# Optimization experiments

Measured on AMD Instinct MI355X. Metric: run time of the kernel, lower is better.

The kernel has to match this reference:

```python
import math
import jax, jax.numpy as jnp
import numpy as np

V_NODES = 100000
N_EDGES = 1600000
EMBED = 768
HID = 256
H = 4
FH = HID // H
L = 2
PE_D = EMBED // 4  # 192
SLOPE = 0.2


def make_pe(max_len, d):
    pos = np.arange(max_len, dtype=np.float32)[:, None]
    div = np.exp(np.arange(0, d, 2, dtype=np.float32) * (-math.log(10000.0) / d))
    pe = np.zeros((max_len, d), dtype=np.float32)
    pe[:, 0::2] = np.sin(pos * div)
    pe[:, 1::2] = np.cos(pos * div)
    return jnp.asarray(pe)


def setup_inputs() -> dict:
    key = jax.random.key(0)
    ks = jax.random.split(key, 24)

    def xavier(k, shape):
        fan_in, fan_out = shape[0], shape[1]
        lim = math.sqrt(6.0 / (fan_in + fan_out))
        return jax.random.uniform(k, shape, jnp.float32, -lim, lim)

    in_proj_dim = EMBED + 2 * PE_D  # 1152
    inp = {
        'row_idx': jax.random.randint(ks[0], (V_NODES,), 0, 256),
        'col_idx': jax.random.randint(ks[1], (V_NODES,), 0, 64),
        'edge_index': jax.random.randint(ks[2], (2, N_EDGES), 0, V_NODES),
        'edge_weight': jax.random.uniform(ks[3], (N_EDGES,), jnp.float32),
        'W_in': xavier(ks[4], (in_proj_dim, HID)),
        'b_in': jnp.zeros((HID,), jnp.float32),
        'ln_g': jnp.ones((HID,), jnp.float32),
        'ln_b': jnp.zeros((HID,), jnp.float32),
        'Wq': jnp.stack([xavier(ks[5 + i], (HID, HID)) for i in range(L)]),
        'bq': jnp.zeros((L, HID), jnp.float32),
        'Wk': jnp.stack([xavier(ks[7 + i], (HID, HID)) for i in range(L)]),
        'bk': jnp.zeros((L, HID), jnp.float32),
        'Wv': jnp.stack([xavier(ks[9 + i], (HID, HID)) for i in range(L)]),
        'bv': jnp.zeros((L, HID), jnp.float32),
        'Wo': jnp.stack([xavier(ks[11 + i], (HID, HID)) for i in range(L)]),
        'bo': jnp.zeros((L, HID), jnp.float32),
        'We': jnp.stack([xavier(ks[13 + i], (1, H)) for i in range(L)]),  # edge_proj weight [1,H]
        'be': jnp.zeros((L, H), jnp.float32),
    }
    return inp


def gat_layer(h, src, tgt, ew, Wq, bq, Wk, bk, Wv, bv, Wo, bo, We, be):
    V = h.shape[0]
    Q = (h @ Wq + bq).reshape(V, H, FH)
    K = (h @ Wk + bk).reshape(V, H, FH)
    Vo = (h @ Wv + bv).reshape(V, H, FH)
    # edge bias: Linear(1,H) on edge_weight, then leaky relu -> [E,H]
    edge_bias = jax.nn.leaky_relu(ew[:, None] * We.reshape(1, H) + be, SLOPE)
    attn_raw = jnp.sum(Q[src] * K[tgt], axis=-1) / math.sqrt(FH) + edge_bias  # [E,H]
    attn_exp = jnp.exp(attn_raw)
    deg = jax.ops.segment_sum(attn_exp, tgt, num_segments=V) + 1e-16  # [V,H]
    attn_norm = attn_exp / deg[tgt]  # [E,H] (dropout is identity at eval)
    msg = Vo[src] * attn_norm[:, :, None] * ew[:, None, None]  # [E,H,FH]
    out = jax.ops.segment_sum(msg, tgt, num_segments=V).reshape(V, H * FH)
    return jax.nn.leaky_relu(out @ Wo + bo, SLOPE)


def reference(row_idx, col_idx, edge_index, edge_weight,
              W_in, b_in, ln_g, ln_b,
              Wq, bq, Wk, bk, Wv, bv, Wo, bo, We, be):
    V = row_idx.shape[0]
    row_pe = make_pe(256, PE_D)
    col_pe = make_pe(64, PE_D)
    cell = jnp.zeros((V, EMBED), jnp.float32)  # cell_embeds are zeros in source
    h = jnp.concatenate([cell, row_pe[row_idx], col_pe[col_idx]], axis=-1)
    # input_proj: Linear -> LayerNorm -> ReLU (dropout identity)
    h = h @ W_in + b_in
    mu = jnp.mean(h, axis=-1, keepdims=True)
    var = jnp.var(h, axis=-1, keepdims=True)
    h = (h - mu) / jnp.sqrt(var + 1e-5) * ln_g + ln_b
    h = jax.nn.relu(h)
    src, tgt = edge_index[0], edge_index[1]
    for i in range(L):
        h = gat_layer(h, src, tgt, edge_weight,
                      Wq[i], bq[i], Wk[i], bk[i], Wv[i], bv[i],
                      Wo[i], bo[i], We[i], be[i])
    return h
```

## Files before the change

kernel.cpp:

```cpp
#include <hip/hip_runtime.h>
#include <hip/hip_bf16.h>
#include <type_traits>
#include <math.h>

typedef __attribute__((ext_vector_type(8))) short bf16x8;
typedef __attribute__((ext_vector_type(4))) float f32x4;

typedef __attribute__((address_space(3))) char       lds_char;
typedef const __attribute__((address_space(1))) char g_char;

__device__ __forceinline__ float bf2f(unsigned int u16) {
    union { unsigned int i; float f; } x; x.i = (u16 & 0xffffu) << 16; return x.f;
}
__device__ __forceinline__ unsigned int f2bf(float f) {
    union { float f; unsigned int i; } x; x.f = f;
    unsigned int i = x.i;
    unsigned int r = i + 0x7fffu + ((i >> 16) & 1u);
    return r >> 16;
}

#define SLOPE 0.2f

__global__ void k_hist(const int* __restrict__ tgt, int* __restrict__ cnt, int E) {
    int i = blockIdx.x * blockDim.x + threadIdx.x;
    if (i < E) atomicAdd(&cnt[tgt[i]], 1);
}

__global__ void __launch_bounds__(1024) k_scan1(const int* __restrict__ in, int* __restrict__ out,
                                                int* __restrict__ bsums, int n) {
    __shared__ int sm[1024];
    int i = blockIdx.x * 1024 + threadIdx.x;
    int v = (i < n) ? in[i] : 0;
    sm[threadIdx.x] = v; __syncthreads();
    for (int ofs = 1; ofs < 1024; ofs <<= 1) {
        int t = (threadIdx.x >= ofs) ? sm[threadIdx.x - ofs] : 0;
        __syncthreads();
        sm[threadIdx.x] += t;
        __syncthreads();
    }
    if (i < n) out[i] = sm[threadIdx.x];
    if (threadIdx.x == 1023) bsums[blockIdx.x] = sm[1023];
}

__global__ void __launch_bounds__(1024) k_scan2(int* bsums, int nb) {
    __shared__ int sm[1024];
    int v = (threadIdx.x < nb) ? bsums[threadIdx.x] : 0;
    sm[threadIdx.x] = v; __syncthreads();
    for (int ofs = 1; ofs < 1024; ofs <<= 1) {
        int t = (threadIdx.x >= ofs) ? sm[threadIdx.x - ofs] : 0;
        __syncthreads();
        sm[threadIdx.x] += t;
        __syncthreads();
    }
    if (threadIdx.x < nb) bsums[threadIdx.x] = sm[threadIdx.x] - v;
}

__global__ void __launch_bounds__(1024) k_scan3(int* __restrict__ out1, const int* __restrict__ bsums,
                                                int* __restrict__ off0, int n) {
    int i = blockIdx.x * 1024 + threadIdx.x;
    if (i < n) out1[i] += bsums[blockIdx.x];
    if (i == 0) off0[0] = 0;
}

__global__ void k_combo(const int* __restrict__ ri, const int* __restrict__ ci,
                        int* __restrict__ combo, int V) {
    int v = blockIdx.x * blockDim.x + threadIdx.x;
    if (v < V) combo[v] = ri[v] * 64 + ci[v];
}

__global__ void k_scatter(const int* __restrict__ ei, const float* __restrict__ ew,
                          const int* __restrict__ off, int* __restrict__ fill,
                          int2* __restrict__ p, int E) {
    int e = blockIdx.x * blockDim.x + threadIdx.x;
    if (e < E) {
        int s = ei[e], t = ei[E + e];
        int pos = off[t] + atomicAdd(&fill[t], 1);
        p[pos] = make_int2(s, __float_as_int(ew[e]));
    }
}

__global__ void __launch_bounds__(256) k_wt(const float* __restrict__ Wq, const float* __restrict__ Wk,
                                            const float* __restrict__ Wv, const float* __restrict__ Wo,
                                            unsigned short* __restrict__ WT) {
    __shared__ float sm[64][65];
    int blk = blockIdx.x;
    int m = blk >> 4, t = blk & 15;
    int tr = t >> 2, tc = t & 3;
    const float* srcs[4] = {Wq, Wk, Wv, Wo};
    const float* W = srcs[m & 3] + (size_t)(m >> 2) * 65536;
    int tid = threadIdx.x;
    for (int i = tid; i < 4096; i += 256) {
        int r = i >> 6, c = i & 63;
        sm[r][c] = W[(size_t)(tr * 64 + r) * 256 + tc * 64 + c];
    }
    __syncthreads();
    for (int i = tid; i < 4096; i += 256) {
        int n = i >> 6, k = i & 63;
        WT[(size_t)(m * 256 + tc * 64 + n) * 256 + tr * 64 + k] = (unsigned short)f2bf(sm[k][n]);
    }
}

__global__ void __launch_bounds__(256) k_bias(const float* __restrict__ bq, const float* __restrict__ bk,
                                              const float* __restrict__ bv, const float* __restrict__ bo,
                                              float* __restrict__ biasF) {
    int m = blockIdx.x, n = threadIdx.x;
    const float* srcs[4] = {bq, bk, bv, bo};
    biasF[m * 256 + n] = srcs[m & 3][(m >> 2) * 256 + n];
}

__global__ void __launch_bounds__(256) k_peproj(const float* __restrict__ W_in, float* __restrict__ AB) {
    __shared__ float pe[192];
    int blk = blockIdx.x;
    bool isA = blk < 256;
    int pos = isA ? blk : blk - 256;
    const float* Wb = W_in + (size_t)(isA ? 768 : 960) * 256;
    int tid = threadIdx.x;
    if (tid < 192) {
        float div = expf(-(float)(tid & ~1) * (logf(10000.0f) / 192.0f));
        float ang = (float)pos * div;
        pe[tid] = (tid & 1) ? cosf(ang) : sinf(ang);
    }
    __syncthreads();
    float acc = 0.f;
    #pragma unroll 8
    for (int d = 0; d < 192; ++d) acc = fmaf(pe[d], Wb[d * 256 + tid], acc);
    AB[blk * 256 + tid] = acc;
}

__global__ void __launch_bounds__(256) k_h0(const float* __restrict__ AB, const float* __restrict__ b_in,
                                            const float* __restrict__ g, const float* __restrict__ b,
                                            unsigned short* __restrict__ h0t) {
    int wid = threadIdx.x >> 6, lane = threadIdx.x & 63;
    int m = blockIdx.x * 4 + wid;
    int r = m >> 6, c = m & 63;
    float4 a  = ((const float4*)(AB + (size_t)r * 256))[lane];
    float4 bb = ((const float4*)(AB + (size_t)(256 + c) * 256))[lane];
    float4 bi = ((const float4*)b_in)[lane];
    float x0 = a.x + bb.x + bi.x, x1 = a.y + bb.y + bi.y;
    float x2 = a.z + bb.z + bi.z, x3 = a.w + bb.w + bi.w;
    float s = x0 + x1 + x2 + x3;
    #pragma unroll
    for (int msk = 1; msk < 64; msk <<= 1) s += __shfl_xor(s, msk);
    float mu = s * (1.f / 256.f);
    float d0 = x0 - mu, d1 = x1 - mu, d2 = x2 - mu, d3 = x3 - mu;
    float sq = d0 * d0 + d1 * d1 + d2 * d2 + d3 * d3;
    #pragma unroll
    for (int msk = 1; msk < 64; msk <<= 1) sq += __shfl_xor(sq, msk);
    float rstd = rsqrtf(sq * (1.f / 256.f) + 1e-5f);
    float4 gv = ((const float4*)g)[lane], bv = ((const float4*)b)[lane];
    float y0 = fmaxf(fmaf(d0 * rstd, gv.x, bv.x), 0.f);
    float y1 = fmaxf(fmaf(d1 * rstd, gv.y, bv.y), 0.f);
    float y2 = fmaxf(fmaf(d2 * rstd, gv.z, bv.z), 0.f);
    float y3 = fmaxf(fmaf(d3 * rstd, gv.w, bv.w), 0.f);
    uint2 o;
    o.x = f2bf(y0) | (f2bf(y1) << 16);
    o.y = f2bf(y2) | (f2bf(y3) << 16);
    *(uint2*)(h0t + (size_t)m * 256 + lane * 4) = o;
}

template <typename TC, bool LEAKY>
__global__ void __launch_bounds__(256) k_mm(const unsigned short* __restrict__ A,
                                            const unsigned short* __restrict__ WT,
                                            const float* __restrict__ bias,
                                            TC* __restrict__ C, int M, int ldc) {
    __shared__ __align__(16) char AsB[16384];
    __shared__ __align__(16) char BsB[16384];
    int tid = threadIdx.x;
    int R0 = blockIdx.x * 128, C0 = blockIdx.y * 128;
    int lane = tid & 63, wave = tid >> 6;
    int wr = (wave >> 1) * 64, wc = (wave & 1) * 64;
    int fr = lane & 15, fq = lane >> 4;
    f32x4 acc[4][4] = {};
    for (int k0 = 0; k0 < 256; k0 += 64) {
        #pragma unroll
        for (int it = 0; it < 4; ++it) {
            int chunk = it * 256 + tid;
            int r = chunk >> 3, cb = (chunk & 7) * 16;
            int sc = cb ^ ((r & 7) << 4);
            int gr = R0 + r;
            if (gr < M)
                __builtin_amdgcn_global_load_lds(
                    (g_char*)((const char*)(A + (size_t)gr * 256 + k0) + sc),
                    (lds_char*)(AsB + (size_t)(it * 256 + wave * 64) * 16), 16, 0, 0);
            __builtin_amdgcn_global_load_lds(
                (g_char*)((const char*)(WT + (size_t)(C0 + r) * 256 + k0) + sc),
                (lds_char*)(BsB + (size_t)(it * 256 + wave * 64) * 16), 16, 0, 0);
        }
        __syncthreads();
        #pragma unroll
        for (int ks = 0; ks < 2; ++ks) {
            bf16x8 af[4], bfv[4];
            #pragma unroll
            for (int mi = 0; mi < 4; ++mi) {
                int r = wr + mi * 16 + fr;
                int kb = ks * 64 + fq * 16;
                af[mi] = *(const bf16x8*)(AsB + r * 128 + (kb ^ ((r & 7) << 4)));
            }
            #pragma unroll
            for (int ni = 0; ni < 4; ++ni) {
                int r = wc + ni * 16 + fr;
                int kb = ks * 64 + fq * 16;
                bfv[ni] = *(const bf16x8*)(BsB + r * 128 + (kb ^ ((r & 7) << 4)));
            }
            #pragma unroll
            for (int mi = 0; mi < 4; ++mi)
                #pragma unroll
                for (int ni = 0; ni < 4; ++ni)
                    acc[mi][ni] = __builtin_amdgcn_mfma_f32_16x16x32_bf16(af[mi], bfv[ni], acc[mi][ni], 0, 0, 0);
        }
        __syncthreads();
    }
    #pragma unroll
    for (int mi = 0; mi < 4; ++mi) {
        #pragma unroll
        for (int r = 0; r < 4; ++r) {
            int row = R0 + wr + mi * 16 + fq * 4 + r;
            if (row >= M) continue;
            #pragma unroll
            for (int ni = 0; ni < 4; ++ni) {
                int col = C0 + wc + ni * 16 + fr;
                float v = acc[mi][ni][r] + bias[col];
                if (LEAKY) v = fmaxf(v, SLOPE * v);
                if constexpr (std::is_same<TC, float>::value) {
                    C[(size_t)row * ldc + col] = v;
                } else {
                    C[(size_t)row * ldc + col] = (unsigned short)f2bf(v);
                }
            }
        }
    }
}

template <bool USE_COMBO>
__global__ void __launch_bounds__(256) k_edge(const int* __restrict__ off, const int2* __restrict__ pedge,
                                              const int* __restrict__ combo,
                                              const unsigned short* __restrict__ QKV,
                                              const float* __restrict__ We_l, const float* __restrict__ be_l,
                                              unsigned short* __restrict__ out, int V) {
    int wid = threadIdx.x >> 6, lane = threadIdx.x & 63;
    int t = blockIdx.x * 4 + wid;
    if (t >= V) return;
    int q = lane & 15, quarter = lane >> 4;
    int h = q >> 2;
    int krow = USE_COMBO ? combo[t] : t;
    uint4 ka = *(const uint4*)(QKV + (size_t)krow * 768 + 256 + q * 16);
    uint4 kb = *(const uint4*)(QKV + (size_t)krow * 768 + 256 + q * 16 + 8);
    float kf[16];
    kf[0] = bf2f(ka.x); kf[1] = bf2f(ka.x >> 16); kf[2] = bf2f(ka.y); kf[3] = bf2f(ka.y >> 16);
    kf[4] = bf2f(ka.z); kf[5] = bf2f(ka.z >> 16); kf[6] = bf2f(ka.w); kf[7] = bf2f(ka.w >> 16);
    kf[8] = bf2f(kb.x); kf[9] = bf2f(kb.x >> 16); kf[10] = bf2f(kb.y); kf[11] = bf2f(kb.y >> 16);
    kf[12] = bf2f(kb.z); kf[13] = bf2f(kb.z >> 16); kf[14] = bf2f(kb.w); kf[15] = bf2f(kb.w >> 16);
    float Weh = We_l[h], beh = be_l[h];
    float n[16];
    #pragma unroll
    for (int j = 0; j < 16; ++j) n[j] = 0.f;
    float den = 0.f;
    int beg = off[t], end = off[t + 1];
    for (int e0 = beg; e0 < end; e0 += 64) {
        int nrem = end - e0; if (nrem > 64) nrem = 64;
        int sv = 0; float wv = 0.f;
        if (lane < nrem) {
            int2 pr = pedge[e0 + lane];
            sv = pr.x;
            wv = __int_as_float(pr.y);
            if (USE_COMBO) sv = combo[sv];
        }
        for (int i = 0; i < nrem; i += 4) {
            int ei = i + quarter;
            bool act = ei < nrem;
            int eidx = act ? ei : (nrem - 1);
            int srow = __shfl(sv, eidx);
            float w  = __shfl(wv, eidx);
            const unsigned short* base = QKV + (size_t)srow * 768 + q * 16;
            uint4 qa = *(const uint4*)base;
            uint4 qb = *(const uint4*)(base + 8);
            uint4 va = *(const uint4*)(base + 512);
            uint4 vb = *(const uint4*)(base + 520);
            float p;
            p = bf2f(qa.x) * kf[0];
            p = fmaf(bf2f(qa.x >> 16), kf[1], p);
            p = fmaf(bf2f(qa.y),       kf[2], p);
            p = fmaf(bf2f(qa.y >> 16), kf[3], p);
            p = fmaf(bf2f(qa.z),       kf[4], p);
            p = fmaf(bf2f(qa.z >> 16), kf[5], p);
            p = fmaf(bf2f(qa.w),       kf[6], p);
            p = fmaf(bf2f(qa.w >> 16), kf[7], p);
            p = fmaf(bf2f(qb.x),       kf[8], p);
            p = fmaf(bf2f(qb.x >> 16), kf[9], p);
            p = fmaf(bf2f(qb.y),       kf[10], p);
            p = fmaf(bf2f(qb.y >> 16), kf[11], p);
            p = fmaf(bf2f(qb.z),       kf[12], p);
            p = fmaf(bf2f(qb.z >> 16), kf[13], p);
            p = fmaf(bf2f(qb.w),       kf[14], p);
            p = fmaf(bf2f(qb.w >> 16), kf[15], p);
            p += __shfl_xor(p, 1);
            p += __shfl_xor(p, 2);
            float bias = fmaf(w, Weh, beh);
            bias = fmaxf(bias, SLOPE * bias);
            float ex = act ? __expf(fmaf(p, 0.125f, bias)) : 0.f;
            den += ex;
            float cc = ex * w;
            n[0]  = fmaf(cc, bf2f(va.x),       n[0]);
            n[1]  = fmaf(cc, bf2f(va.x >> 16), n[1]);
            n[2]  = fmaf(cc, bf2f(va.y),       n[2]);
            n[3]  = fmaf(cc, bf2f(va.y >> 16), n[3]);
            n[4]  = fmaf(cc, bf2f(va.z),       n[4]);
            n[5]  = fmaf(cc, bf2f(va.z >> 16), n[5]);
            n[6]  = fmaf(cc, bf2f(va.w),       n[6]);
            n[7]  = fmaf(cc, bf2f(va.w >> 16), n[7]);
            n[8]  = fmaf(cc, bf2f(vb.x),       n[8]);
            n[9]  = fmaf(cc, bf2f(vb.x >> 16), n[9]);
            n[10] = fmaf(cc, bf2f(vb.y),       n[10]);
            n[11] = fmaf(cc, bf2f(vb.y >> 16), n[11]);
            n[12] = fmaf(cc, bf2f(vb.z),       n[12]);
            n[13] = fmaf(cc, bf2f(vb.z >> 16), n[13]);
            n[14] = fmaf(cc, bf2f(vb.w),       n[14]);
            n[15] = fmaf(cc, bf2f(vb.w >> 16), n[15]);
        }
    }
    den += __shfl_xor(den, 16);
    den += __shfl_xor(den, 32);
    #pragma unroll
    for (int j = 0; j < 16; ++j) {
        n[j] += __shfl_xor(n[j], 16);
        n[j] += __shfl_xor(n[j], 32);
    }
    float inv = 1.f / (den + 1e-16f);
    if (quarter == 0) {
        uint4 o0, o1;
        o0.x = f2bf(n[0] * inv)  | (f2bf(n[1] * inv) << 16);
        o0.y = f2bf(n[2] * inv)  | (f2bf(n[3] * inv) << 16);
        o0.z = f2bf(n[4] * inv)  | (f2bf(n[5] * inv) << 16);
        o0.w = f2bf(n[6] * inv)  | (f2bf(n[7] * inv) << 16);
        o1.x = f2bf(n[8] * inv)  | (f2bf(n[9] * inv) << 16);
        o1.y = f2bf(n[10] * inv) | (f2bf(n[11] * inv) << 16);
        o1.z = f2bf(n[12] * inv) | (f2bf(n[13] * inv) << 16);
        o1.w = f2bf(n[14] * inv) | (f2bf(n[15] * inv) << 16);
        *(uint4*)(out + (size_t)t * 256 + q * 16) = o0;
        *(uint4*)(out + (size_t)t * 256 + q * 16 + 8) = o1;
    }
}

extern "C" void kernel_launch(void* const* d_in, const int* in_sizes, int n_in,
                              void* d_out, int out_size, void* d_ws, size_t ws_size,
                              hipStream_t stream) {
    const int*   row_idx = (const int*)d_in[0];
    const int*   col_idx = (const int*)d_in[1];
    const int*   ei      = (const int*)d_in[2];
    const float* ew      = (const float*)d_in[3];
    const float* W_in    = (const float*)d_in[4];
    const float* b_in    = (const float*)d_in[5];
    const float* ln_g    = (const float*)d_in[6];
    const float* ln_b    = (const float*)d_in[7];
    const float* Wq      = (const float*)d_in[8];
    const float* bq      = (const float*)d_in[9];
    const float* Wk      = (const float*)d_in[10];
    const float* bk      = (const float*)d_in[11];
    const float* Wv      = (const float*)d_in[12];
    const float* bv      = (const float*)d_in[13];
    const float* Wo      = (const float*)d_in[14];
    const float* bo      = (const float*)d_in[15];
    const float* We      = (const float*)d_in[16];
    const float* be      = (const float*)d_in[17];

    const int V = in_sizes[0];
    const int E = in_sizes[3];
    const int NC = 16384;

    char* w = (char*)d_ws;
    size_t o = 0;
    auto alloc = [&](size_t bytes) -> char* {
        char* p = w + o;
        o = (o + bytes + 255) & ~(size_t)255;
        return p;
    };
    int*   cnt     = (int*)alloc((size_t)V * 4);
    int*   fill    = (int*)alloc((size_t)V * 4);
    int*   csr_off = (int*)alloc((size_t)(V + 1) * 4);
    int*   bsums   = (int*)alloc(1024 * 4);
    int2*  csrP    = (int2*)alloc((size_t)E * 8);
    int*   combo   = (int*)alloc((size_t)V * 4);
    float* AB      = (float*)alloc((size_t)320 * 256 * 4);
    unsigned short* WT    = (unsigned short*)alloc((size_t)2048 * 256 * 2);
    float*          biasF = (float*)alloc((size_t)2048 * 4);
    unsigned short* h0t   = (unsigned short*)alloc((size_t)NC * 256 * 2);
    unsigned short* QKV1  = (unsigned short*)alloc((size_t)NC * 768 * 2);
    unsigned short* out_e = (unsigned short*)alloc((size_t)V * 256 * 2);
    unsigned short* h1    = (unsigned short*)alloc((size_t)V * 256 * 2);
    unsigned short* QKV2  = (unsigned short*)alloc((size_t)V * 768 * 2);

    hipMemsetAsync(cnt, 0, (size_t)V * 4, stream);
    hipMemsetAsync(fill, 0, (size_t)V * 4, stream);

    int eb = (E + 255) / 256;
    int nscan = (V + 1023) / 1024;
    k_hist<<<eb, 256, 0, stream>>>(ei + E, cnt, E);
    k_scan1<<<nscan, 1024, 0, stream>>>(cnt, csr_off + 1, bsums, V);
    k_scan2<<<1, 1024, 0, stream>>>(bsums, nscan);
    k_scan3<<<nscan, 1024, 0, stream>>>(csr_off + 1, bsums, csr_off, V);
    k_combo<<<(V + 255) / 256, 256, 0, stream>>>(row_idx, col_idx, combo, V);
    k_scatter<<<eb, 256, 0, stream>>>(ei, ew, csr_off, fill, csrP, E);

    k_wt<<<128, 256, 0, stream>>>(Wq, Wk, Wv, Wo, WT);
    k_bias<<<8, 256, 0, stream>>>(bq, bk, bv, bo, biasF);
    k_peproj<<<320, 256, 0, stream>>>(W_in, AB);
    k_h0<<<NC / 4, 256, 0, stream>>>(AB, b_in, ln_g, ln_b, h0t);

    dim3 g1(NC / 128, 6);
    k_mm<unsigned short, false><<<g1, 256, 0, stream>>>(h0t, WT, biasF, QKV1, NC, 768);

    int tb = (V + 3) / 4;
    k_edge<true><<<tb, 256, 0, stream>>>(csr_off, csrP, combo, QKV1, We, be, out_e, V);

    int mb = (V + 127) / 128;
    dim3 go(mb, 2);
    dim3 gqkv(mb, 6);
    k_mm<unsigned short, true><<<go, 256, 0, stream>>>(out_e, WT + (size_t)768 * 256, biasF + 768, h1, V, 256);
    k_mm<unsigned short, false><<<gqkv, 256, 0, stream>>>(h1, WT + (size_t)1024 * 256, biasF + 1024, QKV2, V, 768);

    k_edge<false><<<tb, 256, 0, stream>>>(csr_off, csrP, combo, QKV2, We + 4, be + 4, out_e, V);

    k_mm<float, true><<<go, 256, 0, stream>>>(out_e, WT + (size_t)1792 * 256, biasF + 1792, (float*)d_out, V, 256);
}
```

Measured before the change: 788.6 us.

## Merge setup kernels into one prep launch and use 256-row GEMM tiles

Folds the weight transpose, bias copy, positional-encoding projection and combo-index kernels into a single multi-role prep kernel, and merges the two memsets into one. It also adds a 512-thread GEMM variant that covers 256 rows per block so each B tile loaded into LDS serves twice as many rows, and uses it for the three full-V matmuls. The single memset relies on cnt and fill sitting next to each other in the allocator, and the larger tile uses more LDS per block, which can lower occupancy.

```diff
diff --git a/kernel.cpp b/kernel.cpp
--- a/kernel.cpp
+++ b/kernel.cpp
@@ -62,12 +62,6 @@
     if (i == 0) off0[0] = 0;
 }
 
-__global__ void k_combo(const int* __restrict__ ri, const int* __restrict__ ci,
-                        int* __restrict__ combo, int V) {
-    int v = blockIdx.x * blockDim.x + threadIdx.x;
-    if (v < V) combo[v] = ri[v] * 64 + ci[v];
-}
-
 __global__ void k_scatter(const int* __restrict__ ei, const float* __restrict__ ew,
                           const int* __restrict__ off, int* __restrict__ fill,
                           int2* __restrict__ p, int E) {
@@ -79,52 +73,56 @@
     }
 }
 
-__global__ void __launch_bounds__(256) k_wt(const float* __restrict__ Wq, const float* __restrict__ Wk,
-                                            const float* __restrict__ Wv, const float* __restrict__ Wo,
-                                            unsigned short* __restrict__ WT) {
+__global__ void __launch_bounds__(256) k_prep(const float* __restrict__ Wq, const float* __restrict__ Wk,
+                                              const float* __restrict__ Wv, const float* __restrict__ Wo,
+                                              unsigned short* __restrict__ WT,
+                                              const float* __restrict__ bq, const float* __restrict__ bk,
+                                              const float* __restrict__ bv, const float* __restrict__ bo,
+                                              float* __restrict__ biasF,
+                                              const float* __restrict__ W_in, float* __restrict__ AB,
+                                              const int* __restrict__ ri, const int* __restrict__ ci,
+                                              int* __restrict__ combo, int V) {
     __shared__ float sm[64][65];
     int blk = blockIdx.x;
-    int m = blk >> 4, t = blk & 15;
-    int tr = t >> 2, tc = t & 3;
-    const float* srcs[4] = {Wq, Wk, Wv, Wo};
-    const float* W = srcs[m & 3] + (size_t)(m >> 2) * 65536;
     int tid = threadIdx.x;
-    for (int i = tid; i < 4096; i += 256) {
-        int r = i >> 6, c = i & 63;
-        sm[r][c] = W[(size_t)(tr * 64 + r) * 256 + tc * 64 + c];
-    }
-    __syncthreads();
-    for (int i = tid; i < 4096; i += 256) {
-        int n = i >> 6, k = i & 63;
-        WT[(size_t)(m * 256 + tc * 64 + n) * 256 + tr * 64 + k] = (unsigned short)f2bf(sm[k][n]);
-    }
-}
-
-__global__ void __launch_bounds__(256) k_bias(const float* __restrict__ bq, const float* __restrict__ bk,
-                                              const float* __restrict__ bv, const float* __restrict__ bo,
-                                              float* __restrict__ biasF) {
-    int m = blockIdx.x, n = threadIdx.x;
-    const float* srcs[4] = {bq, bk, bv, bo};
-    biasF[m * 256 + n] = srcs[m & 3][(m >> 2) * 256 + n];
-}
-
-__global__ void __launch_bounds__(256) k_peproj(const float* __restrict__ W_in, float* __restrict__ AB) {
-    __shared__ float pe[192];
-    int blk = blockIdx.x;
-    bool isA = blk < 256;
-    int pos = isA ? blk : blk - 256;
-    const float* Wb = W_in + (size_t)(isA ? 768 : 960) * 256;
-    int tid = threadIdx.x;
-    if (tid < 192) {
-        float div = expf(-(float)(tid & ~1) * (logf(10000.0f) / 192.0f));
-        float ang = (float)pos * div;
-        pe[tid] = (tid & 1) ? cosf(ang) : sinf(ang);
-    }
-    __syncthreads();
-    float acc = 0.f;
-    #pragma unroll 8
-    for (int d = 0; d < 192; ++d) acc = fmaf(pe[d], Wb[d * 256 + tid], acc);
-    AB[blk * 256 + tid] = acc;
+    if (blk < 128) {
+        int m = blk >> 4, t = blk & 15;
+        int tr = t >> 2, tc = t & 3;
+        const float* srcs[4] = {Wq, Wk, Wv, Wo};
+        const float* W = srcs[m & 3] + (size_t)(m >> 2) * 65536;
+        for (int i = tid; i < 4096; i += 256) {
+            int r = i >> 6, c = i & 63;
+            sm[r][c] = W[(size_t)(tr * 64 + r) * 256 + tc * 64 + c];
+        }
+        __syncthreads();
+        for (int i = tid; i < 4096; i += 256) {
+            int n = i >> 6, k = i & 63;
+            WT[(size_t)(m * 256 + tc * 64 + n) * 256 + tr * 64 + k] = (unsigned short)f2bf(sm[k][n]);
+        }
+    } else if (blk < 136) {
+        int m = blk - 128;
+        const float* srcs[4] = {bq, bk, bv, bo};
+        biasF[m * 256 + tid] = srcs[m & 3][(m >> 2) * 256 + tid];
+    } else if (blk < 456) {
+        int b2 = blk - 136;
+        bool isA = b2 < 256;
+        int pos = isA ? b2 : b2 - 256;
+        const float* Wb = W_in + (size_t)(isA ? 768 : 960) * 256;
+        float* pe = &sm[0][0];
+        if (tid < 192) {
+            float div = expf(-(float)(tid & ~1) * (logf(10000.0f) / 192.0f));
+            float ang = (float)pos * div;
+            pe[tid] = (tid & 1) ? cosf(ang) : sinf(ang);
+        }
+        __syncthreads();
+        float acc = 0.f;
+        #pragma unroll 8
+        for (int d = 0; d < 192; ++d) acc = fmaf(pe[d], Wb[d * 256 + tid], acc);
+        AB[b2 * 256 + tid] = acc;
+    } else {
+        int v = (blk - 456) * 256 + tid;
+        if (v < V) combo[v] = ri[v] * 64 + ci[v];
+    }
 }
 
 __global__ void __launch_bounds__(256) k_h0(const float* __restrict__ AB, const float* __restrict__ b_in,
@@ -185,6 +183,85 @@
             __builtin_amdgcn_global_load_lds(
                 (g_char*)((const char*)(WT + (size_t)(C0 + r) * 256 + k0) + sc),
                 (lds_char*)(BsB + (size_t)(it * 256 + wave * 64) * 16), 16, 0, 0);
+        }
+        __syncthreads();
+        #pragma unroll
+        for (int ks = 0; ks < 2; ++ks) {
+            bf16x8 af[4], bfv[4];
+            #pragma unroll
+            for (int mi = 0; mi < 4; ++mi) {
+                int r = wr + mi * 16 + fr;
+                int kb = ks * 64 + fq * 16;
+                af[mi] = *(const bf16x8*)(AsB + r * 128 + (kb ^ ((r & 7) << 4)));
+            }
+            #pragma unroll
+            for (int ni = 0; ni < 4; ++ni) {
+                int r = wc + ni * 16 + fr;
+                int kb = ks * 64 + fq * 16;
+                bfv[ni] = *(const bf16x8*)(BsB + r * 128 + (kb ^ ((r & 7) << 4)));
+            }
+            #pragma unroll
+            for (int mi = 0; mi < 4; ++mi)
+                #pragma unroll
+                for (int ni = 0; ni < 4; ++ni)
+                    acc[mi][ni] = __builtin_amdgcn_mfma_f32_16x16x32_bf16(af[mi], bfv[ni], acc[mi][ni], 0, 0, 0);
+        }
+        __syncthreads();
+    }
+    #pragma unroll
+    for (int mi = 0; mi < 4; ++mi) {
+        #pragma unroll
+        for (int r = 0; r < 4; ++r) {
+            int row = R0 + wr + mi * 16 + fq * 4 + r;
+            if (row >= M) continue;
+            #pragma unroll
+            for (int ni = 0; ni < 4; ++ni) {
+                int col = C0 + wc + ni * 16 + fr;
+                float v = acc[mi][ni][r] + bias[col];
+                if (LEAKY) v = fmaxf(v, SLOPE * v);
+                if constexpr (std::is_same<TC, float>::value) {
+                    C[(size_t)row * ldc + col] = v;
+                } else {
+                    C[(size_t)row * ldc + col] = (unsigned short)f2bf(v);
+                }
+            }
+        }
+    }
+}
+
+template <typename TC, bool LEAKY>
+__global__ void __launch_bounds__(512) k_mm256(const unsigned short* __restrict__ A,
+                                               const unsigned short* __restrict__ WT,
+                                               const float* __restrict__ bias,
+                                               TC* __restrict__ C, int M, int ldc) {
+    __shared__ __align__(16) char AsB[32768];
+    __shared__ __align__(16) char BsB[16384];
+    int tid = threadIdx.x;
+    int lane = tid & 63, wave = tid >> 6;
+    int R0 = blockIdx.x * 256, C0 = blockIdx.y * 128;
+    int wr = (wave >> 1) * 64, wc = (wave & 1) * 64;
+    int fr = lane & 15, fq = lane >> 4;
+    f32x4 acc[4][4] = {};
+    for (int k0 = 0; k0 < 256; k0 += 64) {
+        #pragma unroll
+        for (int it = 0; it < 4; ++it) {
+            int chunk = it * 512 + tid;
+            int r = chunk >> 3, cb = (chunk & 7) * 16;
+            int sc = cb ^ ((r & 7) << 4);
+            int gr = R0 + r;
+            if (gr < M)
+                __builtin_amdgcn_global_load_lds(
+                    (g_char*)((const char*)(A + (size_t)gr * 256 + k0) + sc),
+                    (lds_char*)(AsB + (size_t)(it * 512 + wave * 64) * 16), 16, 0, 0);
+        }
+        #pragma unroll
+        for (int it = 0; it < 2; ++it) {
+            int chunk = it * 512 + tid;
+            int r = chunk >> 3, cb = (chunk & 7) * 16;
+            int sc = cb ^ ((r & 7) << 4);
+            __builtin_amdgcn_global_load_lds(
+                (g_char*)((const char*)(WT + (size_t)(C0 + r) * 256 + k0) + sc),
+                (lds_char*)(BsB + (size_t)(it * 512 + wave * 64) * 16), 16, 0, 0);
         }
         __syncthreads();
         #pragma unroll
@@ -389,21 +466,19 @@
     unsigned short* h1    = (unsigned short*)alloc((size_t)V * 256 * 2);
     unsigned short* QKV2  = (unsigned short*)alloc((size_t)V * 768 * 2);
 
-    hipMemsetAsync(cnt, 0, (size_t)V * 4, stream);
-    hipMemsetAsync(fill, 0, (size_t)V * 4, stream);
+    hipMemsetAsync(cnt, 0, (size_t)2 * V * 4 + 256, stream);
 
     int eb = (E + 255) / 256;
     int nscan = (V + 1023) / 1024;
+    int prep_blocks = 456 + (V + 255) / 256;
+    k_prep<<<prep_blocks, 256, 0, stream>>>(Wq, Wk, Wv, Wo, WT, bq, bk, bv, bo, biasF,
+                                            W_in, AB, row_idx, col_idx, combo, V);
     k_hist<<<eb, 256, 0, stream>>>(ei + E, cnt, E);
     k_scan1<<<nscan, 1024, 0, stream>>>(cnt, csr_off + 1, bsums, V);
     k_scan2<<<1, 1024, 0, stream>>>(bsums, nscan);
     k_scan3<<<nscan, 1024, 0, stream>>>(csr_off + 1, bsums, csr_off, V);
-    k_combo<<<(V + 255) / 256, 256, 0, stream>>>(row_idx, col_idx, combo, V);
     k_scatter<<<eb, 256, 0, stream>>>(ei, ew, csr_off, fill, csrP, E);
 
-    k_wt<<<128, 256, 0, stream>>>(Wq, Wk, Wv, Wo, WT);
-    k_bias<<<8, 256, 0, stream>>>(bq, bk, bv, bo, biasF);
-    k_peproj<<<320, 256, 0, stream>>>(W_in, AB);
     k_h0<<<NC / 4, 256, 0, stream>>>(AB, b_in, ln_g, ln_b, h0t);
 
     dim3 g1(NC / 128, 6);
@@ -412,13 +487,13 @@
     int tb = (V + 3) / 4;
     k_edge<true><<<tb, 256, 0, stream>>>(csr_off, csrP, combo, QKV1, We, be, out_e, V);
 
-    int mb = (V + 127) / 128;
-    dim3 go(mb, 2);
-    dim3 gqkv(mb, 6);
-    k_mm<unsigned short, true><<<go, 256, 0, stream>>>(out_e, WT + (size_t)768 * 256, biasF + 768, h1, V, 256);
-    k_mm<unsigned short, false><<<gqkv, 256, 0, stream>>>(h1, WT + (size_t)1024 * 256, biasF + 1024, QKV2, V, 768);
+    int mb256 = (V + 255) / 256;
+    dim3 go(mb256, 2);
+    dim3 gqkv(mb256, 6);
+    k_mm256<unsigned short, true><<<go, 512, 0, stream>>>(out_e, WT + (size_t)768 * 256, biasF + 768, h1, V, 256);
+    k_mm256<unsigned short, false><<<gqkv, 512, 0, stream>>>(h1, WT + (size_t)1024 * 256, biasF + 1024, QKV2, V, 768);
 
     k_edge<false><<<tb, 256, 0, stream>>>(csr_off, csrP, combo, QKV2, We + 4, be + 4, out_e, V);
 
-    k_mm<float, true><<<go, 256, 0, stream>>>(out_e, WT + (size_t)1792 * 256, biasF + 1792, (float*)d_out, V, 256);
-}
+    k_mm256<float, true><<<go, 512, 0, stream>>>(out_e, WT + (size_t)1792 * 256, biasF + 1792, (float*)d_out, V, 256);
+}
```

Result: slower. 823.6 us (+4.4%).
